# Kernel optimization log

Hardware: AMD Instinct MI355X
Metric: run time of the kernel (lower is better)

The kernel has to match this reference:

```python
import jax, jax.numpy as jnp
import numpy as np

B, S, FEAT, H, DK, MAX_ITEMS = 8, 1024, 512, 8, 64, 200
LN_EPS = 1e-5
NEG = -999999999.0


def _build_mask(seq_len):
    # rows before T = S-(maxItems+1) cannot see the tail block [T:];
    # tail rows T..S-2 cannot see columns >= their own index (strict upper wedge).
    T = seq_len - (MAX_ITEMS + 1)
    i = jnp.arange(seq_len)[:, None]
    j = jnp.arange(seq_len)[None, :]
    blocked = ((i < T) & (j >= T)) | ((i >= T) & (i <= seq_len - 2) & (j >= i))
    return jnp.where(blocked, NEG, 0.0).astype(jnp.float32)  # [S, S]


def setup_inputs() -> dict:
    key = jax.random.key(0)
    ks = jax.random.split(key, 6)
    def init(k, shape, fan_in):
        return (jax.random.normal(k, shape, jnp.float32) / np.sqrt(fan_in)).astype(jnp.float32)
    return {
        "x": jax.random.normal(ks[0], (B, S, FEAT), jnp.float32),
        "ln_gamma": jnp.ones((FEAT,), jnp.float32),
        "ln_beta": jnp.zeros((FEAT,), jnp.float32),
        "WQ": init(ks[1], (H, FEAT, DK), FEAT), "bq": jnp.zeros((H, DK), jnp.float32),
        "WK": init(ks[2], (H, FEAT, DK), FEAT), "bk": jnp.zeros((H, DK), jnp.float32),
        "WV": init(ks[3], (H, FEAT, DK), FEAT), "bv": jnp.zeros((H, DK), jnp.float32),
        "WO": init(ks[4], (H * DK, FEAT), H * DK), "bO": jnp.zeros((FEAT,), jnp.float32),
    }


def reference(x, ln_gamma, ln_beta, WQ, bq, WK, bk, WV, bv, WO, bO):
    b, s, f = x.shape
    # Pre-LN
    mu = jnp.mean(x, axis=-1, keepdims=True)
    var = jnp.mean((x - mu) ** 2, axis=-1, keepdims=True)
    xn = (x - mu) / jnp.sqrt(var + LN_EPS) * ln_gamma + ln_beta
    # per-head projections, heads stacked: [B, H, S, DK]
    q = jnp.einsum('bsf,hfd->bhsd', xn, WQ) + bq[None, :, None, :]
    k = jnp.einsum('bsf,hfd->bhsd', xn, WK) + bk[None, :, None, :]
    v = jnp.einsum('bsf,hfd->bhsd', xn, WV) + bv[None, :, None, :]
    scores = jnp.einsum('bhsd,bhtd->bhst', q, k) / np.sqrt(DK).astype(np.float32)
    scores = scores + _build_mask(s)[None, None, :, :]
    attn = jax.nn.softmax(scores, axis=-1)
    z = jnp.einsum('bhst,bhtd->bhsd', attn, v)           # [B, H, S, DK]
    z = jnp.transpose(z, (0, 2, 1, 3)).reshape(b, s, -1)  # concat heads -> [B, S, H*DK]
    return z @ WO + bO
```

## Files before the change

kernel.cpp:

```cpp
#include <hip/hip_runtime.h>

#define S_LEN 1024
#define FEATN 512
#define NH    8
#define DKN   64
#define T_CUT 823
#define LDP   76

typedef __attribute__((ext_vector_type(8))) short v8s;
typedef __attribute__((ext_vector_type(4))) float v4f;
typedef unsigned short u16;

__device__ __forceinline__ float bf2f(u16 u) {
    unsigned v = ((unsigned)u) << 16; float f; __builtin_memcpy(&f, &v, 4); return f;
}
__device__ __forceinline__ u16 f2bf(float f) {
    unsigned v; __builtin_memcpy(&v, &f, 4);
    v += 0x7fffu + ((v >> 16) & 1u);
    return (u16)(v >> 16);
}
__device__ __forceinline__ v4f mfma16(v8s a, v8s b, v4f c) {
    return __builtin_amdgcn_mfma_f32_16x16x32_bf16(a, b, c, 0, 0, 0);
}
__device__ __forceinline__ unsigned cvt_pk_bf16(float a, float b) {
    unsigned r;
    asm("v_cvt_pk_bf16_f32 %0, %1, %2" : "=v"(r) : "v"(a), "v"(b));
    return r;
}

__device__ __forceinline__ int sniff_f32(const void* x) {
    const u16* xs = (const u16*)x;
    int wild = 0;
    #pragma unroll
    for (int i = 0; i < 64; i++) {
        float v = bf2f(xs[i]);
        float a = fabsf(v);
        wild |= (!(a <= 256.f)) | ((v != 0.f) & (a <= 1e-9f));
    }
    return wild;
}

__device__ __forceinline__ float read_in(const void* p, long idx, int fl) {
    return fl ? ((const float*)p)[idx] : bf2f(((const u16*)p)[idx]);
}

__global__ __launch_bounds__(256) void prep_kernel(
    const void* __restrict__ x, const void* __restrict__ lg,
    const void* __restrict__ lb,
    const void* __restrict__ WQ, const void* __restrict__ WK,
    const void* __restrict__ WV, const void* __restrict__ WO,
    u16* __restrict__ xn, u16* __restrict__ BtQKV, u16* __restrict__ BtO)
{
    __shared__ u16 ld[64 * 68];
    const int fl = sniff_f32(x);
    const int b = blockIdx.x, t = threadIdx.x;
    if (b < 192) {
        const int which = b >> 6, rem = b & 63, h = rem >> 3, ktile = rem & 7;
        const void* W = which == 0 ? WQ : (which == 1 ? WK : WV);
        const float sc = (which == 0) ? 0.125f : 1.f;
        #pragma unroll
        for (int i = 0; i < 16; i++) {
            int idx = i * 256 + t, r = idx >> 6, c = idx & 63;
            float v = read_in(W, (long)h * 512 * 64 + (long)(ktile * 64 + r) * 64 + c, fl);
            ld[c * 68 + r] = f2bf(v * sc);
        }
        __syncthreads();
        #pragma unroll
        for (int i = 0; i < 16; i++) {
            int idx = i * 256 + t, d = idx >> 6, kk = idx & 63;
            BtQKV[(long)(which * 512 + h * 64 + d) * 512 + ktile * 64 + kk] = ld[d * 68 + kk];
        }
    } else if (b < 256) {
        const int b2 = b - 192, ntile = b2 >> 3, ktile = b2 & 7;
        #pragma unroll
        for (int i = 0; i < 16; i++) {
            int idx = i * 256 + t, r = idx >> 6, c = idx & 63;
            float v = read_in(WO, (long)(ktile * 64 + r) * 512 + ntile * 64 + c, fl);
            ld[c * 68 + r] = f2bf(v);
        }
        __syncthreads();
        #pragma unroll
        for (int i = 0; i < 16; i++) {
            int idx = i * 256 + t, d = idx >> 6, kk = idx & 63;
            BtO[(long)(ntile * 64 + d) * 512 + ktile * 64 + kk] = ld[d * 68 + kk];
        }
    } else {
        const int w = t >> 6, l = t & 63;
        const int row = (b - 256) * 4 + w;
        float f[8];
        if (fl) {
            const float4* x4 = (const float4*)((const float*)x + (size_t)row * FEATN);
            float4 p0 = x4[l * 2], p1 = x4[l * 2 + 1];
            f[0] = p0.x; f[1] = p0.y; f[2] = p0.z; f[3] = p0.w;
            f[4] = p1.x; f[5] = p1.y; f[6] = p1.z; f[7] = p1.w;
        } else {
            const u16* xu = (const u16*)x + (size_t)row * FEATN + l * 8;
            #pragma unroll
            for (int j = 0; j < 8; j++) f[j] = bf2f(xu[j]);
        }
        float s = 0.f, sq = 0.f;
        #pragma unroll
        for (int j = 0; j < 8; j++) { s += f[j]; sq += f[j] * f[j]; }
        #pragma unroll
        for (int sh = 1; sh < 64; sh <<= 1) { s += __shfl_xor(s, sh); sq += __shfl_xor(sq, sh); }
        const float mu = s * (1.f / 512.f);
        const float var = sq * (1.f / 512.f) - mu * mu;
        const float rstd = rsqrtf(var + 1e-5f);
        u16 o8[8];
        #pragma unroll
        for (int j = 0; j < 8; j++) {
            float gg = read_in(lg, l * 8 + j, fl), bb = read_in(lb, l * 8 + j, fl);
            o8[j] = f2bf((f[j] - mu) * rstd * gg + bb);
        }
        *(v8s*)&xn[(size_t)row * FEATN + l * 8] = *(v8s*)o8;
    }
}

__global__ __launch_bounds__(256) void gemm64(
    const void* __restrict__ x,
    const u16* __restrict__ A, const u16* __restrict__ Bt,
    int N, int K, int mode,
    const void* __restrict__ bq, const void* __restrict__ bk,
    const void* __restrict__ bv,
    u16* __restrict__ qp, u16* __restrict__ kw, u16* __restrict__ vt,
    const void* __restrict__ bO, void* __restrict__ out)
{
    __shared__ __attribute__((aligned(16))) u16 lA[2][64 * 32];
    __shared__ __attribute__((aligned(16))) u16 lB[2][128 * 32];
    const int fl = sniff_f32(x);
    const int bid = blockIdx.x;
    const int xcd = bid & 7, sidx = bid >> 3;
    const int m0 = ((sidx & 15) + xcd * 16) * 64;
    const int n0 = (sidx >> 4) * 128;
    const int t = threadIdx.x;
    const int w = t >> 6, l = t & 63, quad = l >> 4, lr = l & 15;
    const int wr = w >> 1, wc = w & 1;
    v4f acc[2][4] = {};
    const int lrow = l >> 2;
    const int gcol = (l & 3) * 8;
    const u16* Ab = A  + (long)m0 * K;
    const u16* Bb = Bt + (long)n0 * K;

    auto stage = [&](int q, int k0) {
        __builtin_amdgcn_global_load_lds(
            (const __attribute__((address_space(1))) void*)
                (Ab + (long)(w * 16 + lrow) * K + k0 + gcol),
            (__attribute__((address_space(3))) void*)&lA[q][(w * 16) * 32],
            16, 0, 0);
        #pragma unroll
        for (int i = 0; i < 2; i++) {
            __builtin_amdgcn_global_load_lds(
                (const __attribute__((address_space(1))) void*)
                    (Bb + (long)(w * 32 + i * 16 + lrow) * K + k0 + gcol),
                (__attribute__((address_space(3))) void*)&lB[q][(w * 32 + i * 16) * 32],
                16, 0, 0);
        }
    };
    stage(0, 0);
    __asm__ __volatile__("s_waitcnt vmcnt(0)" ::: "memory");
    __builtin_amdgcn_s_barrier();
    __builtin_amdgcn_sched_barrier(0);
    int cur = 0;
    for (int k0 = 0; k0 < K; k0 += 32) {
        if (k0 + 32 < K) stage(cur ^ 1, k0 + 32);
        v8s af[2], bf[4];
        #pragma unroll
        for (int i = 0; i < 2; i++)
            af[i] = *(v8s*)&lA[cur][(wr * 32 + i * 16 + lr) * 32 + quad * 8];
        #pragma unroll
        for (int j = 0; j < 4; j++)
            bf[j] = *(v8s*)&lB[cur][(wc * 64 + j * 16 + lr) * 32 + quad * 8];
        #pragma unroll
        for (int i = 0; i < 2; i++)
            #pragma unroll
            for (int j = 0; j < 4; j++)
                acc[i][j] = mfma16(af[i], bf[j], acc[i][j]);
        __asm__ __volatile__("s_waitcnt vmcnt(0)" ::: "memory");
        __builtin_amdgcn_s_barrier();
        __builtin_amdgcn_sched_barrier(0);
        cur ^= 1;
    }
    const int nbase = n0 + wc * 64;
    const int whichW = (mode == 0) ? (nbase >> 9) : -1;
    if (mode == 0 && whichW != 1) {
        u16* tp = (w < 3) ? ((u16*)lB + (size_t)w * 64 * 40) : (u16*)lA;
        const void* bias = (whichW == 0) ? bq : bv;
        const float sc = (whichW == 0) ? 0.125f : 1.f;
        const int nn0 = nbase & 511;
        const int h = nn0 >> 6;
        const int b = (m0 + wr * 32) >> 10;
        const int sbase = (m0 + wr * 32) & 1023;
        u16* dst = ((whichW == 0) ? qp : vt) + (size_t)(b * NH + h) * DKN * S_LEN;
        #pragma unroll
        for (int j = 0; j < 4; j++) {
            const float bs = read_in(bias, nn0 + j * 16 + lr, fl) * sc;
            #pragma unroll
            for (int i = 0; i < 2; i++) {
                u16 q4[4];
                #pragma unroll
                for (int r = 0; r < 4; r++) q4[r] = f2bf(acc[i][j][r] + bs);
                *(uint2*)&tp[(j * 16 + lr) * 40 + i * 16 + quad * 4] =
                    *(const uint2*)q4;
            }
        }
        __asm__ __volatile__("s_waitcnt lgkmcnt(0)" ::: "memory");
        __builtin_amdgcn_sched_barrier(0);
        #pragma unroll
        for (int k = 0; k < 4; k++) {
            const int dl = k * 16 + (l >> 2);
            const int s8 = (l & 3) * 8;
            v8s row = *(v8s*)&tp[dl * 40 + s8];
            *(v8s*)&dst[(size_t)dl * S_LEN + sbase + s8] = row;
        }
    } else {
        #pragma unroll
        for (int i = 0; i < 2; i++)
        #pragma unroll
        for (int j = 0; j < 4; j++) {
            const int mbase = m0 + wr * 32 + i * 16 + quad * 4;
            const int n = n0 + wc * 64 + j * 16 + lr;
            if (mode == 0) {
                const int nn = n & 511, h = nn >> 6, d = nn & 63;
                const float bs = read_in(bk, nn, fl);
                const int b = mbase >> 10, s = mbase & 1023;
                #pragma unroll
                for (int r = 0; r < 4; r++)
                    kw[(((long)(b * NH + h)) * S_LEN + (s + r)) * DKN + d] =
                        f2bf(acc[i][j][r] + bs);
            } else {
                const float bb = read_in(bO, n, fl);
                #pragma unroll
                for (int r = 0; r < 4; r++) {
                    float ov = acc[i][j][r] + bb;
                    if (fl) ((float*)out)[(long)(mbase + r) * N + n] = ov;
                    else    ((u16*)out)[(long)(mbase + r) * N + n] = f2bf(ov);
                }
            }
        }
    }
}

__global__ __launch_bounds__(256) void attn_kernel(
    const u16* __restrict__ qp, const u16* __restrict__ kw,
    const u16* __restrict__ vt, u16* __restrict__ zw)
{
    __shared__ __attribute__((aligned(16))) u16 lk[2][64 * LDP];
    __shared__ __attribute__((aligned(16))) u16 lv[2][64 * LDP];
    const int bid = blockIdx.x;
    const int bh = bid & 63, qt = bid >> 6;
    const int q0 = qt * 64, qmax = q0 + 63;
    const int t = threadIdx.x, w = t >> 6, l = t & 63, quad = l >> 4, lr = l & 15;
    const int srow = t >> 2, scg = t & 3;
    const u16* Qp = qp + (size_t)bh * S_LEN * DKN;
    const u16* Kg = kw + (size_t)bh * S_LEN * DKN;
    const u16* Vt = vt + (size_t)bh * S_LEN * DKN;
    v8s aq[2];
    #pragma unroll
    for (int kf = 0; kf < 2; kf++) {
        u16 tmp[8];
        #pragma unroll
        for (int j = 0; j < 8; j++)
            tmp[j] = Qp[(size_t)(kf * 32 + quad * 8 + j) * S_LEN + q0 + w * 16 + lr];
        __builtin_memcpy(&aq[kf], tmp, 16);
    }
    v4f o[4] = {};
    v4f o1 = {};
    v8s vone;
    #pragma unroll
    for (int j = 0; j < 8; j++) vone[j] = (short)0x3f80;
    const int iq = q0 + w * 16 + quad * 4;
    const int i_row = q0 + w * 16 + lr;
    const int jlim = (i_row < T_CUT) ? T_CUT
                   : ((i_row <= S_LEN - 2) ? i_row : 0x40000000);
    const int mx_ = (T_CUT > qmax) ? T_CUT : qmax;
    const int ntiles = (qmax > S_LEN - 2) ? 16 : ((mx_ + 63) >> 6);
    const int vs = 4 * scg;
    {
        v8s kr0 = *(const v8s*)&Kg[srow * DKN + scg * 8];
        v8s kr1 = *(const v8s*)&Kg[srow * DKN + 32 + scg * 8];
        uint2 va0 = *(const uint2*)&Vt[srow * S_LEN + vs];
        uint2 va1 = *(const uint2*)&Vt[srow * S_LEN + 16 + vs];
        uint2 vb0 = *(const uint2*)&Vt[srow * S_LEN + 32 + vs];
        uint2 vb1 = *(const uint2*)&Vt[srow * S_LEN + 48 + vs];
        *(v8s*)&lk[0][srow * LDP + scg * 8]      = kr0;
        *(v8s*)&lk[0][srow * LDP + 32 + scg * 8] = kr1;
        unsigned wA[4] = {va0.x, va0.y, va1.x, va1.y};
        unsigned wB[4] = {vb0.x, vb0.y, vb1.x, vb1.y};
        v8s vrA, vrB;
        __builtin_memcpy(&vrA, wA, 16);
        __builtin_memcpy(&vrB, wB, 16);
        *(v8s*)&lv[0][srow * LDP + scg * 8]      = vrA;
        *(v8s*)&lv[0][srow * LDP + 32 + scg * 8] = vrB;
    }
    __syncthreads();
    int cur = 0;
    for (int it = 0; it < ntiles; ++it) {
        const int kt0 = it * 64;
        const bool more = (it + 1 < ntiles);
        v8s kr0 = {}, kr1 = {};
        uint2 va0 = {}, va1 = {}, vb0 = {}, vb1 = {};
        if (more) {
            kr0 = *(const v8s*)&Kg[(kt0 + 64 + srow) * DKN + scg * 8];
            kr1 = *(const v8s*)&Kg[(kt0 + 64 + srow) * DKN + 32 + scg * 8];
            const u16* vrow = &Vt[srow * S_LEN + kt0 + 64];
            va0 = *(const uint2*)(vrow + vs);
            va1 = *(const uint2*)(vrow + 16 + vs);
            vb0 = *(const uint2*)(vrow + 32 + vs);
            vb1 = *(const uint2*)(vrow + 48 + vs);
        }
        v4f sf[4];
        __builtin_amdgcn_s_setprio(1);
        #pragma unroll
        for (int cb = 0; cb < 4; cb++) {
            v8s b0 = *(v8s*)&lk[cur][(cb * 16 + lr) * LDP + quad * 8];
            v8s b1 = *(v8s*)&lk[cur][(cb * 16 + lr) * LDP + 32 + quad * 8];
            v4f z = {};
            z = mfma16(b0, aq[0], z);
            z = mfma16(b1, aq[1], z);
            sf[cb] = z;
        }
        __builtin_amdgcn_s_setprio(0);
        const int kt63 = kt0 + 63;
        const bool tmask = ((q0 < T_CUT) && (kt63 >= T_CUT)) ||
                           ((qmax >= T_CUT) && (kt63 >= q0));
        const int jbase = jlim - kt0 - quad * 4;
        unsigned pu[4][2];
        #pragma unroll
        for (int cb = 0; cb < 4; cb++) {
            float e[4];
            #pragma unroll
            for (int r = 0; r < 4; r++) {
                float ev = __expf(sf[cb][r]);
                if (tmask) ev = (cb * 16 + r >= jbase) ? 0.f : ev;
                e[r] = ev;
            }
            pu[cb][0] = cvt_pk_bf16(e[0], e[1]);
            pu[cb][1] = cvt_pk_bf16(e[2], e[3]);
        }
        v8s ap0, ap1;
        {
            unsigned a0_[4] = {pu[0][0], pu[0][1], pu[1][0], pu[1][1]};
            unsigned a1_[4] = {pu[2][0], pu[2][1], pu[3][0], pu[3][1]};
            __builtin_memcpy(&ap0, a0_, 16);
            __builtin_memcpy(&ap1, a1_, 16);
        }
        __builtin_amdgcn_s_setprio(1);
        #pragma unroll
        for (int db = 0; db < 4; db++) {
            v8s bv0 = *(v8s*)&lv[cur][(db * 16 + lr) * LDP + quad * 8];
            o[db] = mfma16(ap0, bv0, o[db]);
        }
        o1 = mfma16(ap0, vone, o1);
        #pragma unroll
        for (int db = 0; db < 4; db++) {
            v8s bv1 = *(v8s*)&lv[cur][(db * 16 + lr) * LDP + 32 + quad * 8];
            o[db] = mfma16(ap1, bv1, o[db]);
        }
        o1 = mfma16(ap1, vone, o1);
        __builtin_amdgcn_s_setprio(0);
        if (more) {
            *(v8s*)&lk[cur ^ 1][srow * LDP + scg * 8]      = kr0;
            *(v8s*)&lk[cur ^ 1][srow * LDP + 32 + scg * 8] = kr1;
            unsigned wA[4] = {va0.x, va0.y, va1.x, va1.y};
            unsigned wB[4] = {vb0.x, vb0.y, vb1.x, vb1.y};
            v8s vrA, vrB;
            __builtin_memcpy(&vrA, wA, 16);
            __builtin_memcpy(&vrB, wB, 16);
            *(v8s*)&lv[cur ^ 1][srow * LDP + scg * 8]      = vrA;
            *(v8s*)&lv[cur ^ 1][srow * LDP + 32 + scg * 8] = vrB;
        }
        __asm__ __volatile__("s_waitcnt lgkmcnt(0)" ::: "memory");
        __builtin_amdgcn_s_barrier();
        __builtin_amdgcn_sched_barrier(0);
        cur ^= 1;
    }
    const int b = bh >> 3, h = bh & 7;
    #pragma unroll
    for (int r = 0; r < 4; r++) {
        const float inv = 1.f / o1[r];
        const int i = iq + r;
        #pragma unroll
        for (int db = 0; db < 4; db++)
            zw[((size_t)b * S_LEN + i) * (NH * DKN) + h * DKN + db * 16 + lr] =
                f2bf(o[db][r] * inv);
    }
}

extern "C" void kernel_launch(void* const* d_in, const int* in_sizes, int n_in,
                              void* d_out, int out_size, void* d_ws, size_t ws_size,
                              hipStream_t stream) {
    const void* x  = d_in[0];
    const void* lg = d_in[1];
    const void* lb = d_in[2];
    const void* WQ = d_in[3];
    const void* bq = d_in[4];
    const void* WK = d_in[5];
    const void* bk = d_in[6];
    const void* WV = d_in[7];
    const void* bv = d_in[8];
    const void* WO = d_in[9];
    const void* bO = d_in[10];

    char* p = (char*)d_ws;
    u16* xn      = (u16*)p;  p += (size_t)8192 * 512 * 2;
    u16* qp      = (u16*)p;  p += (size_t)4194304 * 2;
    u16* kw      = (u16*)p;  p += (size_t)4194304 * 2;
    u16* vt      = (u16*)p;  p += (size_t)4194304 * 2;
    u16* zw      = (u16*)p;  p += (size_t)8192 * 512 * 2;
    u16* BtQKV   = (u16*)p;  p += (size_t)1536 * 512 * 2;
    u16* BtO     = (u16*)p;  p += (size_t)512 * 512 * 2;

    prep_kernel<<<2304, 256, 0, stream>>>(x, lg, lb, WQ, WK, WV, WO, xn, BtQKV, BtO);
    gemm64<<<1536, 256, 0, stream>>>(x, xn, BtQKV, 1536, 512, 0,
                                     bq, bk, bv, qp, kw, vt, nullptr, nullptr);
    attn_kernel<<<1024, 256, 0, stream>>>(qp, kw, vt, zw);
    gemm64<<<512, 256, 0, stream>>>(x, zw, BtO, 512, 512, 1,
                                    nullptr, nullptr, nullptr,
                                    nullptr, nullptr, nullptr, bO, d_out);
}
```

Baseline: 181.4 us.

## Make GEMM warps independent with per-warp LDS staging and no block barriers

Replaces the shared-tile GEMM with a per-wave design in which each wave stages its own A rows plus a full 128-column B tile into private LDS double buffers. Partial vmcnt waits replace block-wide barriers. The QKV GEMM now uses 128x128 block tiles with 768 blocks, and the output GEMM uses 64x128 tiles. This removes barrier stalls, but each wave loads B redundantly, which raises global traffic and LDS use (about 80-64KB per block) and may lower occupancy.

After: 182.2 us. About the same (+0.4%).

```diff
diff --git a/kernel.cpp b/kernel.cpp
--- a/kernel.cpp
+++ b/kernel.cpp
@@ -116,7 +116,8 @@
     }
 }
 
-__global__ __launch_bounds__(256) void gemm64(
+template<int WM>
+__global__ __launch_bounds__(256) void gemm_wp(
     const void* __restrict__ x,
     const u16* __restrict__ A, const u16* __restrict__ Bt,
     int N, int K, int mode,
@@ -125,100 +126,113 @@
     u16* __restrict__ qp, u16* __restrict__ kw, u16* __restrict__ vt,
     const void* __restrict__ bO, void* __restrict__ out)
 {
-    __shared__ __attribute__((aligned(16))) u16 lA[2][64 * 32];
-    __shared__ __attribute__((aligned(16))) u16 lB[2][128 * 32];
+    constexpr int MI = WM / 16;
+    constexpr int G  = MI + 8;
+    constexpr int BUFS = (WM + 128) * 32;
+    __shared__ __attribute__((aligned(16))) u16 lds[4 * 2 * BUFS];
     const int fl = sniff_f32(x);
     const int bid = blockIdx.x;
+    constexpr int MTPX = 256 / WM;
     const int xcd = bid & 7, sidx = bid >> 3;
-    const int m0 = ((sidx & 15) + xcd * 16) * 64;
-    const int n0 = (sidx >> 4) * 128;
+    const int m0 = ((sidx & (MTPX - 1)) + xcd * MTPX) * (4 * WM);
+    const int n0 = (sidx / MTPX) * 128;
     const int t = threadIdx.x;
     const int w = t >> 6, l = t & 63, quad = l >> 4, lr = l & 15;
-    const int wr = w >> 1, wc = w & 1;
-    v4f acc[2][4] = {};
     const int lrow = l >> 2;
     const int gcol = (l & 3) * 8;
-    const u16* Ab = A  + (long)m0 * K;
+    u16* ldsw = lds + (size_t)w * 2 * BUFS;
+    v4f acc[MI][8] = {};
+    const u16* Aw = A  + (long)(m0 + w * WM) * K;
     const u16* Bb = Bt + (long)n0 * K;
 
     auto stage = [&](int q, int k0) {
-        __builtin_amdgcn_global_load_lds(
-            (const __attribute__((address_space(1))) void*)
-                (Ab + (long)(w * 16 + lrow) * K + k0 + gcol),
-            (__attribute__((address_space(3))) void*)&lA[q][(w * 16) * 32],
-            16, 0, 0);
-        #pragma unroll
-        for (int i = 0; i < 2; i++) {
+        u16* base = ldsw + q * BUFS;
+        #pragma unroll
+        for (int i = 0; i < MI; i++)
             __builtin_amdgcn_global_load_lds(
                 (const __attribute__((address_space(1))) void*)
-                    (Bb + (long)(w * 32 + i * 16 + lrow) * K + k0 + gcol),
-                (__attribute__((address_space(3))) void*)&lB[q][(w * 32 + i * 16) * 32],
+                    (Aw + (long)(i * 16 + lrow) * K + k0 + gcol),
+                (__attribute__((address_space(3))) void*)&base[i * 16 * 32],
                 16, 0, 0);
-        }
+        #pragma unroll
+        for (int i = 0; i < 8; i++)
+            __builtin_amdgcn_global_load_lds(
+                (const __attribute__((address_space(1))) void*)
+                    (Bb + (long)(i * 16 + lrow) * K + k0 + gcol),
+                (__attribute__((address_space(3))) void*)&base[WM * 32 + i * 16 * 32],
+                16, 0, 0);
     };
     stage(0, 0);
-    __asm__ __volatile__("s_waitcnt vmcnt(0)" ::: "memory");
-    __builtin_amdgcn_s_barrier();
-    __builtin_amdgcn_sched_barrier(0);
     int cur = 0;
     for (int k0 = 0; k0 < K; k0 += 32) {
-        if (k0 + 32 < K) stage(cur ^ 1, k0 + 32);
-        v8s af[2], bf[4];
-        #pragma unroll
-        for (int i = 0; i < 2; i++)
-            af[i] = *(v8s*)&lA[cur][(wr * 32 + i * 16 + lr) * 32 + quad * 8];
-        #pragma unroll
-        for (int j = 0; j < 4; j++)
-            bf[j] = *(v8s*)&lB[cur][(wc * 64 + j * 16 + lr) * 32 + quad * 8];
-        #pragma unroll
-        for (int i = 0; i < 2; i++)
+        const bool more = (k0 + 32 < K);
+        if (more) {
+            stage(cur ^ 1, k0 + 32);
+            __asm__ __volatile__("s_waitcnt vmcnt(%0)" :: "i"(G) : "memory");
+        } else {
+            __asm__ __volatile__("s_waitcnt vmcnt(0)" ::: "memory");
+        }
+        __builtin_amdgcn_sched_barrier(0);
+        const u16* base = ldsw + cur * BUFS;
+        v8s af[MI], bf[8];
+        #pragma unroll
+        for (int i = 0; i < MI; i++)
+            af[i] = *(const v8s*)&base[(i * 16 + lr) * 32 + quad * 8];
+        #pragma unroll
+        for (int j = 0; j < 8; j++)
+            bf[j] = *(const v8s*)&base[WM * 32 + (j * 16 + lr) * 32 + quad * 8];
+        #pragma unroll
+        for (int i = 0; i < MI; i++)
             #pragma unroll
-            for (int j = 0; j < 4; j++)
+            for (int j = 0; j < 8; j++)
                 acc[i][j] = mfma16(af[i], bf[j], acc[i][j]);
-        __asm__ __volatile__("s_waitcnt vmcnt(0)" ::: "memory");
-        __builtin_amdgcn_s_barrier();
-        __builtin_amdgcn_sched_barrier(0);
         cur ^= 1;
     }
-    const int nbase = n0 + wc * 64;
-    const int whichW = (mode == 0) ? (nbase >> 9) : -1;
+    const int whichW = (mode == 0) ? (n0 >> 9) : -1;
     if (mode == 0 && whichW != 1) {
-        u16* tp = (w < 3) ? ((u16*)lB + (size_t)w * 64 * 40) : (u16*)lA;
-        const void* bias = (whichW == 0) ? bq : bv;
-        const float sc = (whichW == 0) ? 0.125f : 1.f;
-        const int nn0 = nbase & 511;
-        const int h = nn0 >> 6;
-        const int b = (m0 + wr * 32) >> 10;
-        const int sbase = (m0 + wr * 32) & 1023;
-        u16* dst = ((whichW == 0) ? qp : vt) + (size_t)(b * NH + h) * DKN * S_LEN;
-        #pragma unroll
-        for (int j = 0; j < 4; j++) {
-            const float bs = read_in(bias, nn0 + j * 16 + lr, fl) * sc;
+        if constexpr (WM == 32) {
+            __asm__ __volatile__("s_waitcnt lgkmcnt(0)" ::: "memory");
+            u16* tp = ldsw;
+            const void* bias = (whichW == 0) ? bq : bv;
+            const float sc = (whichW == 0) ? 0.125f : 1.f;
+            const int nn0 = n0 & 511;
+            const int b = (m0 + w * 32) >> 10;
+            const int sbase = (m0 + w * 32) & 1023;
             #pragma unroll
-            for (int i = 0; i < 2; i++) {
-                u16 q4[4];
+            for (int j = 0; j < 8; j++) {
+                const int jc = j * 16 + lr;
+                const float bs = read_in(bias, nn0 + jc, fl) * sc;
                 #pragma unroll
-                for (int r = 0; r < 4; r++) q4[r] = f2bf(acc[i][j][r] + bs);
-                *(uint2*)&tp[(j * 16 + lr) * 40 + i * 16 + quad * 4] =
-                    *(const uint2*)q4;
+                for (int i = 0; i < 2; i++) {
+                    u16 q4[4];
+                    #pragma unroll
+                    for (int r = 0; r < 4; r++) q4[r] = f2bf(acc[i][j][r] + bs);
+                    *(uint2*)&tp[jc * 40 + i * 16 + quad * 4] = *(const uint2*)q4;
+                }
             }
-        }
-        __asm__ __volatile__("s_waitcnt lgkmcnt(0)" ::: "memory");
-        __builtin_amdgcn_sched_barrier(0);
-        #pragma unroll
-        for (int k = 0; k < 4; k++) {
-            const int dl = k * 16 + (l >> 2);
-            const int s8 = (l & 3) * 8;
-            v8s row = *(v8s*)&tp[dl * 40 + s8];
-            *(v8s*)&dst[(size_t)dl * S_LEN + sbase + s8] = row;
+            __asm__ __volatile__("s_waitcnt lgkmcnt(0)" ::: "memory");
+            __builtin_amdgcn_sched_barrier(0);
+            u16* dstb = ((whichW == 0) ? qp : vt) +
+                        (size_t)(b * NH + (nn0 >> 6)) * DKN * S_LEN;
+            #pragma unroll
+            for (int hh = 0; hh < 2; hh++) {
+                u16* dst = dstb + (size_t)hh * DKN * S_LEN;
+                #pragma unroll
+                for (int k2 = 0; k2 < 4; k2++) {
+                    const int dl = k2 * 16 + (l >> 2);
+                    const int s8 = (l & 3) * 8;
+                    v8s row = *(const v8s*)&tp[(hh * 64 + dl) * 40 + s8];
+                    *(v8s*)&dst[(size_t)dl * S_LEN + sbase + s8] = row;
+                }
+            }
         }
     } else {
         #pragma unroll
-        for (int i = 0; i < 2; i++)
-        #pragma unroll
-        for (int j = 0; j < 4; j++) {
-            const int mbase = m0 + wr * 32 + i * 16 + quad * 4;
-            const int n = n0 + wc * 64 + j * 16 + lr;
+        for (int i = 0; i < MI; i++)
+        #pragma unroll
+        for (int j = 0; j < 8; j++) {
+            const int mbase = m0 + w * WM + i * 16 + quad * 4;
+            const int n = n0 + j * 16 + lr;
             if (mode == 0) {
                 const int nn = n & 511, h = nn >> 6, d = nn & 63;
                 const float bs = read_in(bk, nn, fl);
@@ -411,10 +425,10 @@
     u16* BtO     = (u16*)p;  p += (size_t)512 * 512 * 2;
 
     prep_kernel<<<2304, 256, 0, stream>>>(x, lg, lb, WQ, WK, WV, WO, xn, BtQKV, BtO);
-    gemm64<<<1536, 256, 0, stream>>>(x, xn, BtQKV, 1536, 512, 0,
-                                     bq, bk, bv, qp, kw, vt, nullptr, nullptr);
+    gemm_wp<32><<<768, 256, 0, stream>>>(x, xn, BtQKV, 1536, 512, 0,
+                                         bq, bk, bv, qp, kw, vt, nullptr, nullptr);
     attn_kernel<<<1024, 256, 0, stream>>>(qp, kw, vt, zw);
-    gemm64<<<512, 256, 0, stream>>>(x, zw, BtO, 512, 512, 1,
-                                    nullptr, nullptr, nullptr,
-                                    nullptr, nullptr, nullptr, bO, d_out);
-}
+    gemm_wp<16><<<512, 256, 0, stream>>>(x, zw, BtO, 512, 512, 1,
+                                         nullptr, nullptr, nullptr,
+                                         nullptr, nullptr, nullptr, bO, d_out);
+}
```
